# Kernel tuning notes

Measured on AMD Instinct MI355X. Metric: run time of the kernel, lower is better.

## Reference

```python
import jax, jax.numpy as jnp
import numpy as np

N = 8192
IN_F = 512
OUT_F = 64
ALPHA = 0.2  # LeakyReLU negative slope
NEG_INF = -9e15


def setup_inputs() -> dict:
    key = jax.random.key(0)
    k1, k2, k3, k4 = jax.random.split(key, 4)
    inp = jax.random.normal(k1, (N, IN_F), dtype=jnp.float32)
    adj = jax.random.randint(k2, (N, N), 0, 2, dtype=jnp.int32)
    W = jax.random.normal(k3, (IN_F, OUT_F), dtype=jnp.float32) * (1.414 * (6.0 / (IN_F + OUT_F)) ** 0.5)
    a = jax.random.normal(k4, (2 * OUT_F, 1), dtype=jnp.float32) * (1.414 * (6.0 / (2 * OUT_F + 1)) ** 0.5)
    return {"input": inp, "adj": adj, "W": W, "a": a}


def reference(input, adj, W, a):
    h = input @ W                      # [N, F]
    F_ = h.shape[1]
    # e_ij = leakyrelu(a[:F].h_i + a[F:].h_j)  (equivalent to the concat form)
    f_src = h @ a[:F_, 0]              # [N]
    f_dst = h @ a[F_:, 0]              # [N]
    e = jax.nn.leaky_relu(f_src[:, None] + f_dst[None, :], negative_slope=ALPHA)  # [N, N]
    att = jnp.where(adj > 0, e, jnp.float32(NEG_INF))
    att = jax.nn.softmax(att, axis=1)  # dropout p is inert in eval mode
    h_prime = att @ h                  # [N, F]
    return jax.nn.elu(h_prime)         # concat=True
```

## Files before the change

### kernel.cpp

```cpp
#include <hip/hip_runtime.h>

#define N_NODES 8192
#define IN_F 512
#define OUT_F 64
#define LOG2E 1.4426950408889634f
#define JSPLIT 8

typedef short bf16x8 __attribute__((ext_vector_type(8)));
typedef float f32x4 __attribute__((ext_vector_type(4)));

__global__ __launch_bounds__(256) void k_gemm(const float* __restrict__ input,
                                              const float* __restrict__ W,
                                              const float* __restrict__ a,
                                              unsigned short* __restrict__ hT,
                                              float* __restrict__ fsrcL,
                                              float* __restrict__ fdstL) {
  const int lane = threadIdx.x & 63;
  const int wv = threadIdx.x >> 6;
  const int r0 = blockIdx.x * 16;
  const int rw = r0 + wv * 4;
  const int c = lane;
  float acc[4] = {0.f, 0.f, 0.f, 0.f};
  const float* Wc = W + c;
  for (int k = 0; k < IN_F; k += 4) {
    float w0 = Wc[(k + 0) * OUT_F];
    float w1 = Wc[(k + 1) * OUT_F];
    float w2 = Wc[(k + 2) * OUT_F];
    float w3 = Wc[(k + 3) * OUT_F];
#pragma unroll
    for (int r = 0; r < 4; r++) {
      float4 x = *(const float4*)(input + (size_t)(rw + r) * IN_F + k);
      acc[r] += x.x * w0 + x.y * w1 + x.z * w2 + x.w * w3;
    }
  }
#pragma unroll
  for (int r = 0; r < 4; r++) {
    float vs = acc[r] * a[c];
    float vd = acc[r] * a[OUT_F + c];
#pragma unroll
    for (int off = 32; off > 0; off >>= 1) {
      vs += __shfl_xor(vs, off, 64);
      vd += __shfl_xor(vd, off, 64);
    }
    if (lane == 0) {
      fsrcL[rw + r] = vs * LOG2E;
      fdstL[rw + r] = vd * LOG2E;
    }
  }
  __shared__ float hs[16][65];
#pragma unroll
  for (int r = 0; r < 4; r++) hs[wv * 4 + r][c] = acc[r];
  __syncthreads();
  {
    const int cc = threadIdx.x >> 2;
    const int q = threadIdx.x & 3;
    unsigned uu[4];
#pragma unroll
    for (int rr = 0; rr < 4; rr++)
      uu[rr] = __float_as_uint(hs[q * 4 + rr][cc]) + 0x8000u;
    uint2 pk;
    pk.x = __builtin_amdgcn_perm(uu[1], uu[0], 0x07060302u);
    pk.y = __builtin_amdgcn_perm(uu[3], uu[2], 0x07060302u);
    *(uint2*)(hT + (size_t)cc * N_NODES + r0 + q * 4) = pk;
  }
}

__global__ __launch_bounds__(256) void k_max(const float* __restrict__ fdstL,
                                             float* __restrict__ ML) {
  float m = -3.0e38f;
  for (int i = threadIdx.x; i < N_NODES; i += 256) m = fmaxf(m, fdstL[i]);
#pragma unroll
  for (int off = 32; off > 0; off >>= 1) m = fmaxf(m, __shfl_xor(m, off, 64));
  __shared__ float sm[4];
  if ((threadIdx.x & 63) == 0) sm[threadIdx.x >> 6] = m;
  __syncthreads();
  if (threadIdx.x == 0) ML[0] = fmaxf(fmaxf(sm[0], sm[1]), fmaxf(sm[2], sm[3]));
}

__global__ __launch_bounds__(256) void k_attn(const int* __restrict__ adj,
                                              const unsigned short* __restrict__ hT,
                                              const float* __restrict__ fsrcL,
                                              const float* __restrict__ fdstL,
                                              const float* __restrict__ MLp,
                                              float* __restrict__ num,
                                              float* __restrict__ den) {
  const int lane = threadIdx.x & 63;
  const int wv = threadIdx.x >> 6;
  const int rb = blockIdx.x >> 3;
  const int js = blockIdx.x & 7;
  const int i0 = rb * 16;
  const int m = lane & 15;
  const int g = lane >> 4;

  const float MLv = MLp[0];
  const float fs = fsrcL[i0 + m];
  const float xm = fs + MLv;
  const float mL = fmaxf(xm, 0.2f * xm);

  f32x4 acc0{}, acc1{}, acc2{}, acc3{};
  float lpart = 0.f;

  const int* adjrow = adj + (size_t)(i0 + m) * N_NODES;
  const unsigned short* hT0 = hT + (size_t)m * N_NODES;

  const int jbeg = js * (N_NODES / JSPLIT) + wv * 256;
  for (int j0 = jbeg; j0 < jbeg + 256; j0 += 64) {
    const int jb0 = j0 + g * 8;
    const int jb1 = j0 + 32 + g * 8;
    int4 a00 = *(const int4*)(adjrow + jb0);
    int4 a01 = *(const int4*)(adjrow + jb0 + 4);
    int4 a10 = *(const int4*)(adjrow + jb1);
    int4 a11 = *(const int4*)(adjrow + jb1 + 4);
    float4 d00 = *(const float4*)(fdstL + jb0);
    float4 d01 = *(const float4*)(fdstL + jb0 + 4);
    float4 d10 = *(const float4*)(fdstL + jb1);
    float4 d11 = *(const float4*)(fdstL + jb1 + 4);
    bf16x8 b00 = *(const bf16x8*)(hT0 + jb0);
    bf16x8 b01 = *(const bf16x8*)(hT0 + (size_t)16 * N_NODES + jb0);
    bf16x8 b02 = *(const bf16x8*)(hT0 + (size_t)32 * N_NODES + jb0);
    bf16x8 b03 = *(const bf16x8*)(hT0 + (size_t)48 * N_NODES + jb0);
    bf16x8 b10 = *(const bf16x8*)(hT0 + jb1);
    bf16x8 b11 = *(const bf16x8*)(hT0 + (size_t)16 * N_NODES + jb1);
    bf16x8 b12 = *(const bf16x8*)(hT0 + (size_t)32 * N_NODES + jb1);
    bf16x8 b13 = *(const bf16x8*)(hT0 + (size_t)48 * N_NODES + jb1);
    {
      const int av[8] = {a00.x, a00.y, a00.z, a00.w, a01.x, a01.y, a01.z, a01.w};
      const float dv[8] = {d00.x, d00.y, d00.z, d00.w, d01.x, d01.y, d01.z, d01.w};
      unsigned u[8];
#pragma unroll
      for (int t = 0; t < 8; t++) {
        float x = fs + dv[t];
        float y = fmaxf(x, 0.2f * x) - mL;
        float p = __builtin_amdgcn_exp2f(y);
        p = av[t] ? p : 0.0f;
        lpart += p;
        u[t] = __float_as_uint(p) + 0x8000u;
      }
      union { unsigned w[4]; bf16x8 v; } pc;
      pc.w[0] = __builtin_amdgcn_perm(u[1], u[0], 0x07060302u);
      pc.w[1] = __builtin_amdgcn_perm(u[3], u[2], 0x07060302u);
      pc.w[2] = __builtin_amdgcn_perm(u[5], u[4], 0x07060302u);
      pc.w[3] = __builtin_amdgcn_perm(u[7], u[6], 0x07060302u);
      acc0 = __builtin_amdgcn_mfma_f32_16x16x32_bf16(pc.v, b00, acc0, 0, 0, 0);
      acc1 = __builtin_amdgcn_mfma_f32_16x16x32_bf16(pc.v, b01, acc1, 0, 0, 0);
      acc2 = __builtin_amdgcn_mfma_f32_16x16x32_bf16(pc.v, b02, acc2, 0, 0, 0);
      acc3 = __builtin_amdgcn_mfma_f32_16x16x32_bf16(pc.v, b03, acc3, 0, 0, 0);
    }
    {
      const int av[8] = {a10.x, a10.y, a10.z, a10.w, a11.x, a11.y, a11.z, a11.w};
      const float dv[8] = {d10.x, d10.y, d10.z, d10.w, d11.x, d11.y, d11.z, d11.w};
      unsigned u[8];
#pragma unroll
      for (int t = 0; t < 8; t++) {
        float x = fs + dv[t];
        float y = fmaxf(x, 0.2f * x) - mL;
        float p = __builtin_amdgcn_exp2f(y);
        p = av[t] ? p : 0.0f;
        lpart += p;
        u[t] = __float_as_uint(p) + 0x8000u;
      }
      union { unsigned w[4]; bf16x8 v; } pc;
      pc.w[0] = __builtin_amdgcn_perm(u[1], u[0], 0x07060302u);
      pc.w[1] = __builtin_amdgcn_perm(u[3], u[2], 0x07060302u);
      pc.w[2] = __builtin_amdgcn_perm(u[5], u[4], 0x07060302u);
      pc.w[3] = __builtin_amdgcn_perm(u[7], u[6], 0x07060302u);
      acc0 = __builtin_amdgcn_mfma_f32_16x16x32_bf16(pc.v, b10, acc0, 0, 0, 0);
      acc1 = __builtin_amdgcn_mfma_f32_16x16x32_bf16(pc.v, b11, acc1, 0, 0, 0);
      acc2 = __builtin_amdgcn_mfma_f32_16x16x32_bf16(pc.v, b12, acc2, 0, 0, 0);
      acc3 = __builtin_amdgcn_mfma_f32_16x16x32_bf16(pc.v, b13, acc3, 0, 0, 0);
    }
  }

  lpart += __shfl_xor(lpart, 16, 64);
  lpart += __shfl_xor(lpart, 32, 64);

  __shared__ float accbuf[4][16][64];
  __shared__ float lbuf[4][16];
#pragma unroll
  for (int r = 0; r < 4; r++) {
    accbuf[wv][g * 4 + r][0 + m]  = acc0[r];
    accbuf[wv][g * 4 + r][16 + m] = acc1[r];
    accbuf[wv][g * 4 + r][32 + m] = acc2[r];
    accbuf[wv][g * 4 + r][48 + m] = acc3[r];
  }
  if (lane < 16) lbuf[wv][lane] = lpart;
  __syncthreads();

#pragma unroll
  for (int q = 0; q < 4; q++) {
    int idx = q * 256 + threadIdx.x;
    int r = idx >> 6, c = idx & 63;
    float ssum = accbuf[0][r][c] + accbuf[1][r][c] + accbuf[2][r][c] + accbuf[3][r][c];
    num[((size_t)js * N_NODES + i0 + r) * OUT_F + c] = ssum;
  }
  if (threadIdx.x < 16) {
    den[(size_t)js * N_NODES + i0 + threadIdx.x] =
        lbuf[0][threadIdx.x] + lbuf[1][threadIdx.x] + lbuf[2][threadIdx.x] + lbuf[3][threadIdx.x];
  }
}

__global__ __launch_bounds__(256) void k_merge(const float* __restrict__ num,
                                               const float* __restrict__ den,
                                               float* __restrict__ out) {
  const int idx = blockIdx.x * 256 + threadIdx.x;
  const int i = idx >> 6;
  float s = 0.f, l = 0.f;
#pragma unroll
  for (int js = 0; js < JSPLIT; js++) {
    s += num[((size_t)js * N_NODES) * OUT_F + idx];
    l += den[(size_t)js * N_NODES + i];
  }
  float v = s / l;
  out[idx] = v > 0.f ? v : __builtin_amdgcn_exp2f(v * LOG2E) - 1.f;
}

extern "C" void kernel_launch(void* const* d_in, const int* in_sizes, int n_in,
                              void* d_out, int out_size, void* d_ws, size_t ws_size,
                              hipStream_t stream) {
  const float* input = (const float*)d_in[0];
  const int* adj = (const int*)d_in[1];
  const float* W = (const float*)d_in[2];
  const float* a = (const float*)d_in[3];
  float* out = (float*)d_out;

  char* ws = (char*)d_ws;
  unsigned short* hT = (unsigned short*)ws;
  float* fsrcL = (float*)(ws + (1u << 20));
  float* fdstL = (float*)(ws + (1u << 20) + 32 * 1024);
  float* ML = (float*)(ws + (1u << 20) + 64 * 1024);
  float* num = (float*)(ws + (2u << 20));
  float* den = (float*)(ws + (20u << 20));

  k_gemm<<<N_NODES / 16, 256, 0, stream>>>(input, W, a, hT, fsrcL, fdstL);
  k_max<<<1, 256, 0, stream>>>(fdstL, ML);
  k_attn<<<(N_NODES / 16) * JSPLIT, 256, 0, stream>>>(adj, hT, fsrcL, fdstL, ML, num, den);
  k_merge<<<N_NODES * OUT_F / 256, 256, 0, stream>>>(num, den, out);
}
```

Measured before the change: 450.3 us.

## Fuse max reduction into GEMM and merge into attention kernel with 8-wave blocks

Removes the single-block max kernel by folding a global max of fdst into the GEMM through an order-preserving atomicMax. It also drops the JSPLIT partial-sum scheme: each 512-thread block now covers all columns for its 16 rows and reduces across its 8 waves in shared memory, then writes the ELU output directly. This removes the merge kernel, the num/den workspace traffic and two launches. The cost is fewer, larger attention blocks (512 of them instead of 4096), which may reduce latency hiding. The LeakyReLU arithmetic is also rewritten in FMA form with precomputed offsets.

```diff
diff --git a/kernel.cpp b/kernel.cpp
--- a/kernel.cpp
+++ b/kernel.cpp
@@ -4,17 +4,25 @@
 #define IN_F 512
 #define OUT_F 64
 #define LOG2E 1.4426950408889634f
-#define JSPLIT 8
 
 typedef short bf16x8 __attribute__((ext_vector_type(8)));
 typedef float f32x4 __attribute__((ext_vector_type(4)));
+
+__device__ __forceinline__ unsigned enc_ord(float f) {
+  unsigned u = __float_as_uint(f);
+  return (u & 0x80000000u) ? ~u : (u | 0x80000000u);
+}
+__device__ __forceinline__ float dec_ord(unsigned u) {
+  return __uint_as_float((u & 0x80000000u) ? (u & 0x7fffffffu) : ~u);
+}
 
 __global__ __launch_bounds__(256) void k_gemm(const float* __restrict__ input,
                                               const float* __restrict__ W,
                                               const float* __restrict__ a,
                                               unsigned short* __restrict__ hT,
                                               float* __restrict__ fsrcL,
-                                              float* __restrict__ fdstL) {
+                                              float* __restrict__ fdstL,
+                                              unsigned* __restrict__ MLe) {
   const int lane = threadIdx.x & 63;
   const int wv = threadIdx.x >> 6;
   const int r0 = blockIdx.x * 16;
@@ -33,6 +41,7 @@
       acc[r] += x.x * w0 + x.y * w1 + x.z * w2 + x.w * w3;
     }
   }
+  float wmax = -3.0e38f;
 #pragma unroll
   for (int r = 0; r < 4; r++) {
     float vs = acc[r] * a[c];
@@ -42,15 +51,21 @@
       vs += __shfl_xor(vs, off, 64);
       vd += __shfl_xor(vd, off, 64);
     }
+    vd *= LOG2E;
+    wmax = fmaxf(wmax, vd);
     if (lane == 0) {
       fsrcL[rw + r] = vs * LOG2E;
-      fdstL[rw + r] = vd * LOG2E;
+      fdstL[rw + r] = vd;
     }
   }
   __shared__ float hs[16][65];
+  __shared__ float smax[4];
+  if (lane == 0) smax[wv] = wmax;
 #pragma unroll
   for (int r = 0; r < 4; r++) hs[wv * 4 + r][c] = acc[r];
   __syncthreads();
+  if (threadIdx.x == 0)
+    atomicMax(MLe, enc_ord(fmaxf(fmaxf(smax[0], smax[1]), fmaxf(smax[2], smax[3]))));
   {
     const int cc = threadIdx.x >> 2;
     const int q = threadIdx.x & 3;
@@ -65,37 +80,24 @@
   }
 }
 
-__global__ __launch_bounds__(256) void k_max(const float* __restrict__ fdstL,
-                                             float* __restrict__ ML) {
-  float m = -3.0e38f;
-  for (int i = threadIdx.x; i < N_NODES; i += 256) m = fmaxf(m, fdstL[i]);
-#pragma unroll
-  for (int off = 32; off > 0; off >>= 1) m = fmaxf(m, __shfl_xor(m, off, 64));
-  __shared__ float sm[4];
-  if ((threadIdx.x & 63) == 0) sm[threadIdx.x >> 6] = m;
-  __syncthreads();
-  if (threadIdx.x == 0) ML[0] = fmaxf(fmaxf(sm[0], sm[1]), fmaxf(sm[2], sm[3]));
-}
-
-__global__ __launch_bounds__(256) void k_attn(const int* __restrict__ adj,
-                                              const unsigned short* __restrict__ hT,
-                                              const float* __restrict__ fsrcL,
-                                              const float* __restrict__ fdstL,
-                                              const float* __restrict__ MLp,
-                                              float* __restrict__ num,
-                                              float* __restrict__ den) {
+__global__ __launch_bounds__(512, 4) void k_attn(const int* __restrict__ adj,
+                                                 const unsigned short* __restrict__ hT,
+                                                 const float* __restrict__ fsrcL,
+                                                 const float* __restrict__ fdstL,
+                                                 const unsigned* __restrict__ MLe,
+                                                 float* __restrict__ out) {
   const int lane = threadIdx.x & 63;
   const int wv = threadIdx.x >> 6;
-  const int rb = blockIdx.x >> 3;
-  const int js = blockIdx.x & 7;
-  const int i0 = rb * 16;
+  const int i0 = blockIdx.x * 16;
   const int m = lane & 15;
   const int g = lane >> 4;
 
-  const float MLv = MLp[0];
+  const float MLv = dec_ord(MLe[0]);
   const float fs = fsrcL[i0 + m];
   const float xm = fs + MLv;
   const float mL = fmaxf(xm, 0.2f * xm);
+  const float fsm = fs - mL;
+  const float f2 = fmaf(0.2f, fs, -mL);
 
   f32x4 acc0{}, acc1{}, acc2{}, acc3{};
   float lpart = 0.f;
@@ -103,8 +105,8 @@
   const int* adjrow = adj + (size_t)(i0 + m) * N_NODES;
   const unsigned short* hT0 = hT + (size_t)m * N_NODES;
 
-  const int jbeg = js * (N_NODES / JSPLIT) + wv * 256;
-  for (int j0 = jbeg; j0 < jbeg + 256; j0 += 64) {
+  const int jbeg = wv * (N_NODES / 8);
+  for (int j0 = jbeg; j0 < jbeg + (N_NODES / 8); j0 += 64) {
     const int jb0 = j0 + g * 8;
     const int jb1 = j0 + 32 + g * 8;
     int4 a00 = *(const int4*)(adjrow + jb0);
@@ -129,8 +131,7 @@
       unsigned u[8];
 #pragma unroll
       for (int t = 0; t < 8; t++) {
-        float x = fs + dv[t];
-        float y = fmaxf(x, 0.2f * x) - mL;
+        float y = fmaxf(fsm + dv[t], fmaf(0.2f, dv[t], f2));
         float p = __builtin_amdgcn_exp2f(y);
         p = av[t] ? p : 0.0f;
         lpart += p;
@@ -152,8 +153,7 @@
       unsigned u[8];
 #pragma unroll
       for (int t = 0; t < 8; t++) {
-        float x = fs + dv[t];
-        float y = fmaxf(x, 0.2f * x) - mL;
+        float y = fmaxf(fsm + dv[t], fmaf(0.2f, dv[t], f2));
         float p = __builtin_amdgcn_exp2f(y);
         p = av[t] ? p : 0.0f;
         lpart += p;
@@ -174,8 +174,8 @@
   lpart += __shfl_xor(lpart, 16, 64);
   lpart += __shfl_xor(lpart, 32, 64);
 
-  __shared__ float accbuf[4][16][64];
-  __shared__ float lbuf[4][16];
+  __shared__ float accbuf[8][16][64];
+  __shared__ float lbuf[8][16];
 #pragma unroll
   for (int r = 0; r < 4; r++) {
     accbuf[wv][g * 4 + r][0 + m]  = acc0[r];
@@ -187,31 +187,19 @@
   __syncthreads();
 
 #pragma unroll
-  for (int q = 0; q < 4; q++) {
-    int idx = q * 256 + threadIdx.x;
+  for (int q = 0; q < 2; q++) {
+    int idx = q * 512 + threadIdx.x;
     int r = idx >> 6, c = idx & 63;
-    float ssum = accbuf[0][r][c] + accbuf[1][r][c] + accbuf[2][r][c] + accbuf[3][r][c];
-    num[((size_t)js * N_NODES + i0 + r) * OUT_F + c] = ssum;
-  }
-  if (threadIdx.x < 16) {
-    den[(size_t)js * N_NODES + i0 + threadIdx.x] =
-        lbuf[0][threadIdx.x] + lbuf[1][threadIdx.x] + lbuf[2][threadIdx.x] + lbuf[3][threadIdx.x];
-  }
-}
-
-__global__ __launch_bounds__(256) void k_merge(const float* __restrict__ num,
-                                               const float* __restrict__ den,
-                                               float* __restrict__ out) {
-  const int idx = blockIdx.x * 256 + threadIdx.x;
-  const int i = idx >> 6;
-  float s = 0.f, l = 0.f;
-#pragma unroll
-  for (int js = 0; js < JSPLIT; js++) {
-    s += num[((size_t)js * N_NODES) * OUT_F + idx];
-    l += den[(size_t)js * N_NODES + i];
-  }
-  float v = s / l;
-  out[idx] = v > 0.f ? v : __builtin_amdgcn_exp2f(v * LOG2E) - 1.f;
+    float ssum = 0.f, ltot = 0.f;
+#pragma unroll
+    for (int w = 0; w < 8; w++) {
+      ssum += accbuf[w][r][c];
+      ltot += lbuf[w][r];
+    }
+    float v = ssum / ltot;
+    out[(size_t)(i0 + r) * OUT_F + c] =
+        v > 0.f ? v : __builtin_amdgcn_exp2f(v * LOG2E) - 1.f;
+  }
 }
 
 extern "C" void kernel_launch(void* const* d_in, const int* in_sizes, int n_in,
@@ -227,12 +215,9 @@
   unsigned short* hT = (unsigned short*)ws;
   float* fsrcL = (float*)(ws + (1u << 20));
   float* fdstL = (float*)(ws + (1u << 20) + 32 * 1024);
-  float* ML = (float*)(ws + (1u << 20) + 64 * 1024);
-  float* num = (float*)(ws + (2u << 20));
-  float* den = (float*)(ws + (20u << 20));
-
-  k_gemm<<<N_NODES / 16, 256, 0, stream>>>(input, W, a, hT, fsrcL, fdstL);
-  k_max<<<1, 256, 0, stream>>>(fdstL, ML);
-  k_attn<<<(N_NODES / 16) * JSPLIT, 256, 0, stream>>>(adj, hT, fsrcL, fdstL, ML, num, den);
-  k_merge<<<N_NODES * OUT_F / 256, 256, 0, stream>>>(num, den, out);
-}
+  unsigned* MLe = (unsigned*)(ws + (1u << 20) + 64 * 1024);
+
+  hipMemsetAsync(MLe, 0, 4, stream);
+  k_gemm<<<N_NODES / 16, 256, 0, stream>>>(input, W, a, hT, fsrcL, fdstL, MLe);
+  k_attn<<<N_NODES / 16, 512, 0, stream>>>(adj, hT, fsrcL, fdstL, MLe, out);
+}
```

Measured after the change: 467.5 us. +3.8%, slower.
